# Performance work log

Measured on AMD Instinct MI355X. Metric: run time of the kernel, lower is better.

The kernel has to match this reference:

```python
import jax, jax.numpy as jnp
import numpy as np

E = 1024   # embd_size
H = 16     # heads_num
DH = E // H
DFF = 4 * E
B, T = 2, 2048


def layer_norm(x, g, b, eps=1e-5):
    mu = jnp.mean(x, axis=-1, keepdims=True)
    var = jnp.var(x, axis=-1, keepdims=True)
    return (x - mu) * jax.lax.rsqrt(var + eps) * g + b


def setup_inputs() -> dict:
    key = jax.random.key(0)
    ks = jax.random.split(key, 12)
    s = 0.02
    return {
        "x": jax.random.normal(ks[0], (B, T, E), dtype=jnp.float32),
        "Wq": jax.random.normal(ks[1], (E, E), dtype=jnp.float32) * s,
        "Wk": jax.random.normal(ks[2], (E, E), dtype=jnp.float32) * s,
        "Wv": jax.random.normal(ks[3], (E, E), dtype=jnp.float32) * s,
        "Wo": jax.random.normal(ks[4], (E, E), dtype=jnp.float32) * s,
        "bo": jnp.zeros((E,), dtype=jnp.float32),
        "W1": jax.random.normal(ks[5], (E, DFF), dtype=jnp.float32) * s,
        "b1": jnp.zeros((DFF,), dtype=jnp.float32),
        "W2": jax.random.normal(ks[6], (DFF, E), dtype=jnp.float32) * s,
        "b2": jnp.zeros((E,), dtype=jnp.float32),
        "g1": jnp.ones((E,), dtype=jnp.float32),
        "be1": jnp.zeros((E,), dtype=jnp.float32),
        "g2": jnp.ones((E,), dtype=jnp.float32),
        "be2": jnp.zeros((E,), dtype=jnp.float32),
    }


def reference(x, Wq, Wk, Wv, Wo, bo, W1, b1, W2, b2, g1, be1, g2, be2):
    Bx, Tx, C = x.shape
    # --- self-attention sublayer ---
    h = layer_norm(x, g1, be1)
    # per-head projections; heads concatenated along output dim == stacked weights
    q = (h @ Wq).reshape(Bx, Tx, H, DH)  # [B,T,H,Dh]
    k = (h @ Wk).reshape(Bx, Tx, H, DH)
    v = (h @ Wv).reshape(Bx, Tx, H, DH)
    # NOTE: original scales by full embd_size**-0.5 (C = x.shape[-1]), not head_size
    scale = C ** (-0.5)
    scores = jnp.einsum("bqhd,bkhd->bhqk", q, k) * scale  # [B,H,T,T]
    mask = jnp.tril(jnp.ones((Tx, Tx), dtype=bool))
    scores = jnp.where(mask, scores, -jnp.inf)
    attn = jax.nn.softmax(scores, axis=-1)
    o = jnp.einsum("bhqk,bkhd->bqhd", attn, v).reshape(Bx, Tx, C)
    sa = o @ Wo + bo
    x = x + sa
    # --- feed-forward sublayer ---
    h2 = layer_norm(x, g2, be2)
    ff = jax.nn.relu(h2 @ W1 + b1) @ W2 + b2
    return x + ff
```

## Files before the change

### kernel.cpp

```cpp
#include <hip/hip_runtime.h>
#include <hip/hip_bf16.h>
#include <math.h>

#define Bn 2
#define Tn 2048
#define En 1024
#define Hn 16
#define DFFn 4096
#define Mn (Bn*Tn)
#define QKVLD 3072

typedef __hip_bfloat16 bf16;
typedef unsigned short u16;
typedef unsigned int u32;
typedef __attribute__((ext_vector_type(8))) short short8;
typedef __attribute__((ext_vector_type(4))) float f32x4;

typedef __attribute__((address_space(1))) const void cg_void;
typedef __attribute__((address_space(3))) void lds_void;

#define QSC 0.0450842200278f

#define HBAR() asm volatile("s_waitcnt lgkmcnt(0)\n\ts_barrier" ::: "memory")

__device__ __forceinline__ u16 f2bf(float f) {
    bf16 h = __float2bfloat16(f);
    u16 u; __builtin_memcpy(&u, &h, 2); return u;
}
__device__ __forceinline__ float bf2f(u16 u) {
    u32 x = ((u32)u) << 16; float f; __builtin_memcpy(&f, &x, 4); return f;
}

__global__ __launch_bounds__(256)
void transpose_w4(const float* __restrict__ s0, const float* __restrict__ s1,
                  const float* __restrict__ s2, const float* __restrict__ s3,
                  u16* __restrict__ d0, u16* __restrict__ d1,
                  u16* __restrict__ d2, u16* __restrict__ d3) {
    const float* src = (blockIdx.z == 0) ? s0 : (blockIdx.z == 1) ? s1
                     : (blockIdx.z == 2) ? s2 : s3;
    u16* dst = (blockIdx.z == 0) ? d0 : (blockIdx.z == 1) ? d1
             : (blockIdx.z == 2) ? d2 : d3;
    __shared__ float t[64][65];
    const int r0 = blockIdx.y * 64, c0 = blockIdx.x * 64;
    const int tr = threadIdx.x >> 6, tc = threadIdx.x & 63;
#pragma unroll
    for (int i = 0; i < 16; i++)
        t[tr + i * 4][tc] = src[(size_t)(r0 + tr + i * 4) * 1024 + c0 + tc];
    __syncthreads();
#pragma unroll
    for (int i = 0; i < 16; i++)
        dst[(size_t)(c0 + tr + i * 4) * 1024 + r0 + tc] = f2bf(t[tc][tr + i * 4]);
}

__global__ __launch_bounds__(256)
void transpose_w(const float* __restrict__ src, u16* __restrict__ dst,
                 int R, int C) {
    __shared__ float t[64][65];
    const int r0 = blockIdx.y * 64, c0 = blockIdx.x * 64;
    const int tr = threadIdx.x >> 6, tc = threadIdx.x & 63;
#pragma unroll
    for (int i = 0; i < 16; i++)
        t[tr + i * 4][tc] = src[(size_t)(r0 + tr + i * 4) * C + c0 + tc];
    __syncthreads();
#pragma unroll
    for (int i = 0; i < 16; i++)
        dst[(size_t)(c0 + tr + i * 4) * R + r0 + tc] = f2bf(t[tc][tr + i * 4]);
}

__global__ __launch_bounds__(256)
void vcopy_t(const u16* __restrict__ QKV, u16* __restrict__ Vg) {
    const int bh = blockIdx.z;
    const int t0 = blockIdx.y * 64;
    __shared__ u16 t[64][65];
    const int tr = threadIdx.x >> 6, tc = threadIdx.x & 63;
    const u16* src = QKV + (size_t)(bh >> 4) * 2048 * QKVLD + 2048 + (bh & 15) * 64;
#pragma unroll
    for (int i = 0; i < 16; i++)
        t[tr + i * 4][tc] = src[(size_t)(t0 + tr + i * 4) * QKVLD + tc];
    __syncthreads();
    u16* dst = Vg + (size_t)bh * 64 * 2048;
#pragma unroll
    for (int i = 0; i < 16; i++)
        dst[(size_t)(tr + i * 4) * 2048 + t0 + tc] = t[tc][tr + i * 4];
}

template<typename AT>
__global__ __launch_bounds__(256)
void ln_kernel(const AT* __restrict__ x, const float* __restrict__ g,
               const float* __restrict__ b, u16* __restrict__ out) {
    const int row = blockIdx.x;
    const int tid = threadIdx.x;
    const AT* xp = x + (size_t)row * En;
    float v[4];
    float s = 0.f, sq = 0.f;
#pragma unroll
    for (int i = 0; i < 4; i++) {
        if constexpr (sizeof(AT) == 2) v[i] = bf2f(xp[tid + i * 256]);
        else                           v[i] = (float)xp[tid + i * 256];
        s += v[i];
        sq += v[i] * v[i];
    }
    __shared__ float rs[256], rq[256];
    rs[tid] = s; rq[tid] = sq;
    __syncthreads();
    for (int st = 128; st > 0; st >>= 1) {
        if (tid < st) { rs[tid] += rs[tid + st]; rq[tid] += rq[tid + st]; }
        __syncthreads();
    }
    const float mu  = rs[0] * (1.0f / En);
    const float var = rq[0] * (1.0f / En) - mu * mu;
    const float inv = rsqrtf(var + 1e-5f);
#pragma unroll
    for (int i = 0; i < 4; i++) {
        const int c = tid + i * 256;
        out[(size_t)row * En + c] = f2bf((v[i] - mu) * inv * g[c] + b[c]);
    }
}

__global__ __launch_bounds__(256)
void ff2_init(const u16* __restrict__ X1, const float* __restrict__ b2,
              float* __restrict__ out) {
    const int row = blockIdx.x;
    const int c = threadIdx.x * 4;
    ushort4 a = *(const ushort4*)&X1[(size_t)row * En + c];
    float4 bb = *(const float4*)&b2[c];
    float4 o;
    o.x = bf2f(a.x) + bb.x;
    o.y = bf2f(a.y) + bb.y;
    o.z = bf2f(a.z) + bb.z;
    o.w = bf2f(a.w) + bb.w;
    *(float4*)&out[(size_t)row * En + c] = o;
}

template<int TN, int HAS_BIAS, int RELU, int SPLITC, int SCQ, int ATOM,
         int SPLITA, int XSWZ>
__global__ __launch_bounds__(512, 2)
void gemm256(const u16* __restrict__ A, const u16* __restrict__ A2, int ldA,
             const u16* __restrict__ Wt, int ldW,
             const float* __restrict__ bias,
             u16* __restrict__ Cout, u16* __restrict__ Cout2,
             float* __restrict__ outF, int ldC, int Kd) {
    constexpr int WGN = (TN == 256) ? 4 : 2;
    constexpr int MF  = (256 / (8 / WGN)) / 16;
    constexpr int NF  = (TN / WGN) / 16;
    __shared__ __align__(16) u16 As[2][256 * 64];
    __shared__ __align__(16) u16 Bs[2][TN * 64];
    const int tid  = threadIdx.x;
    const int lane = tid & 63, wv = tid >> 6;
    const int quad = lane >> 4, l16 = lane & 15;
    const int wr = wv / WGN, wc = wv % WGN;
    const int lr8 = lane >> 3;
    const int gcg = (lane & 7) ^ lr8;

    int bx = blockIdx.x, by = blockIdx.y, bz = blockIdx.z;
    if (XSWZ) {
        const int GX = gridDim.x, GY = gridDim.y;
        const int L = (bz * GY + by) * GX + bx;
        const int xcd = L & 7, slot = L >> 3;
        const int p = slot / GX;
        bx = slot - p * GX;
        const int yz = p * 8 + xcd;
        by = yz & (GY - 1);
        bz = yz >> 4;
    }

    const int m0 = by * 256, n0 = bx * TN;
    const u16* Ap = (SPLITA && ATOM && bz) ? A2 : A;
    const int kbase = ATOM ? bz * Kd : 0;

    f32x4 acc[MF][NF] = {};

    auto stage = [&](int buf, int kt) {
#pragma unroll
        for (int i = 0; i < 4; i++) {
            const int rbase = wv * 32 + i * 8;
            __builtin_amdgcn_global_load_lds(
                (cg_void*)(const void*)&Ap[(size_t)(m0 + rbase + lr8) * ldA + kt + gcg * 8],
                (lds_void*)(void*)&As[buf][rbase * 64], 16, 0, 0);
        }
#pragma unroll
        for (int i = 0; i < TN / 64; i++) {
            const int rbase = wv * (TN / 8) + i * 8;
            __builtin_amdgcn_global_load_lds(
                (cg_void*)(const void*)&Wt[(size_t)(n0 + rbase + lr8) * ldW + kbase + kt + gcg * 8],
                (lds_void*)(void*)&Bs[buf][rbase * 64], 16, 0, 0);
        }
    };
    auto compute = [&](int buf) {
        const int swz = l16 & 7;
#pragma unroll
        for (int ks = 0; ks < 2; ks++) {
            short8 a[MF], b[NF];
#pragma unroll
            for (int mf = 0; mf < MF; mf++)
                a[mf] = *(const short8*)&As[buf][(wr * (MF * 16) + mf * 16 + l16) * 64 +
                         (((ks * 4 + quad) ^ swz) * 8)];
#pragma unroll
            for (int nf = 0; nf < NF; nf++)
                b[nf] = *(const short8*)&Bs[buf][(wc * 64 + nf * 16 + l16) * 64 +
                         (((ks * 4 + quad) ^ swz) * 8)];
#pragma unroll
            for (int mf = 0; mf < MF; mf++)
#pragma unroll
                for (int nf = 0; nf < NF; nf++)
                    acc[mf][nf] = __builtin_amdgcn_mfma_f32_16x16x32_bf16(
                        a[mf], b[nf], acc[mf][nf], 0, 0, 0);
        }
    };

    stage(0, 0);
    asm volatile("s_waitcnt vmcnt(0)" ::: "memory");
    __builtin_amdgcn_s_barrier();
    const int NT = Kd >> 6;
    for (int t = 0; t < NT; ++t) {
        const int cur = t & 1;
        if (t + 1 < NT) stage(cur ^ 1, (t + 1) * 64);
        compute(cur);
        asm volatile("s_waitcnt vmcnt(0) lgkmcnt(0)" ::: "memory");
        __builtin_amdgcn_s_barrier();
    }

    const float qscale = (SCQ && n0 < 1024) ? QSC : 1.0f;
#pragma unroll
    for (int mf = 0; mf < MF; mf++) {
#pragma unroll
        for (int r = 0; r < 4; r++) {
            const int gm = m0 + wr * (MF * 16) + mf * 16 + quad * 4 + r;
#pragma unroll
            for (int nf = 0; nf < NF; nf++) {
                const int gn = n0 + wc * 64 + nf * 16 + l16;
                const int cn = SPLITC ? (gn & 2047) : gn;
                float c = acc[mf][nf][r];
                if (HAS_BIAS) c += bias[gn];
                if (RELU) c = fmaxf(c, 0.f);
                if (SCQ) c *= qscale;
                if (ATOM) {
                    atomicAdd(&outF[(size_t)gm * ldC + gn], c);
                } else {
                    u16* Cp = (SPLITC && gn >= 2048) ? Cout2 : Cout;
                    Cp[(size_t)gm * ldC + cn] = f2bf(c);
                }
            }
        }
    }
}

template<int TM, int HAS_BIAS, int RELU, int RES, int OUT_F32, int SCQ,
         int SPLITC, int SPLITA, int ATOM = 0, int XSWZ = 0, int PIPE = 0>
__global__ __launch_bounds__(256)
void gemm_bt(const u16* __restrict__ A, const u16* __restrict__ A2, int ldA,
             const u16* __restrict__ Wt, int ldW,
             const float* __restrict__ bias, const void* __restrict__ res,
             void* __restrict__ Cout, void* __restrict__ Cout2,
             int ldC, int Kd) {
    constexpr int IF = TM / 32;
    constexpr int RB = 1;
    __shared__ __align__(16) u16 As[RB][TM * 32];
    __shared__ __align__(16) u16 Bs[RB][128 * 32];
    const int tid  = threadIdx.x;
    const int lane = tid & 63, wv = tid >> 6;
    const int quad = lane >> 4, l16 = lane & 15;

    int bx = blockIdx.x, by = blockIdx.y, bz = blockIdx.z;
    if (XSWZ) {
        const int GX = gridDim.x, GY = gridDim.y;
        const int L = (bz * GY + by) * GX + bx;
        const int xcd = L & 7, slot = L >> 3;
        const int p = slot / GX;
        bx = slot - p * GX;
        const int yz = p * 8 + xcd;
        by = yz & (GY - 1);
        bz = yz >> __builtin_ctz(GY);
    }

    const int m0 = by * TM, n0 = bx * 128;
    const int rw = (wv >> 1) * (TM / 2), cw = (wv & 1) * 64;
    const int lr  = lane >> 2;
    const int gsw = ((lane & 3) ^ ((lane >> 3) & 3)) * 8;
    const int psw = (quad ^ ((l16 >> 1) & 3)) * 8;

    f32x4 acc[IF][4] = {};

    auto stage = [&](int buf, int kt) {
        const u16* Ap = (SPLITA && kt >= 2048) ? A2 : A;
        const int  kk = SPLITA ? (kt & 2047) : kt;
#pragma unroll
        for (int t = 0; t < TM / 64; t++) {
            const int row = wv * (TM / 4) + t * 16;
            __builtin_amdgcn_global_load_lds(
                (cg_void*)(const void*)&Ap[(size_t)(m0 + row + lr) * ldA + kk + gsw],
                (lds_void*)(void*)&As[buf][row * 32], 16, 0, 0);
        }
#pragma unroll
        for (int t = 0; t < 2; t++) {
            const int row = wv * 32 + t * 16;
            __builtin_amdgcn_global_load_lds(
                (cg_void*)(const void*)&Wt[(size_t)(n0 + row + lr) * ldW + kt + gsw],
                (lds_void*)(void*)&Bs[buf][row * 32], 16, 0, 0);
        }
    };
    auto compute = [&](int buf) {
        short8 af[IF], bfr[4];
#pragma unroll
        for (int i = 0; i < IF; i++)
            af[i] = *(const short8*)&As[buf][(rw + i * 16 + l16) * 32 + psw];
#pragma unroll
        for (int j = 0; j < 4; j++)
            bfr[j] = *(const short8*)&Bs[buf][(cw + j * 16 + l16) * 32 + psw];
#pragma unroll
        for (int i = 0; i < IF; i++)
#pragma unroll
            for (int j = 0; j < 4; j++)
                acc[i][j] = __builtin_amdgcn_mfma_f32_16x16x32_bf16(
                    af[i], bfr[j], acc[i][j], 0, 0, 0);
    };

    const int kbase = ATOM ? bz * Kd : 0;
    for (int kt = kbase; kt < kbase + Kd; kt += 32) {
        __syncthreads();
        stage(0, kt);
        __syncthreads();
        compute(0);
    }

    const float qscale = (SCQ && n0 < 1024) ? QSC : 1.0f;
    void* Cp = (SPLITC && n0 >= 2048) ? Cout2 : Cout;
#pragma unroll
    for (int i = 0; i < IF; i++) {
#pragma unroll
        for (int r = 0; r < 4; r++) {
            const int gm = m0 + rw + i * 16 + quad * 4 + r;
#pragma unroll
            for (int j = 0; j < 4; j++) {
                const int gn = n0 + cw + j * 16 + l16;
                const int cn = SPLITC ? (gn & 2047) : gn;
                float c = acc[i][j][r];
                if (HAS_BIAS) c += bias[gn];
                if (RELU) c = fmaxf(c, 0.f);
                if (RES == 1) c += ((const float*)res)[(size_t)gm * ldC + cn];
                if (RES == 2) c += bf2f(((const u16*)res)[(size_t)gm * ldC + cn]);
                if (SCQ) c *= qscale;
                if (ATOM) {
                    atomicAdd(&((float*)Cp)[(size_t)gm * ldC + cn], c);
                } else if (OUT_F32) {
                    ((float*)Cp)[(size_t)gm * ldC + cn] = c;
                } else {
                    ((u16*)Cp)[(size_t)gm * ldC + cn] = f2bf(c);
                }
            }
        }
    }
}

__global__ __launch_bounds__(256)
void flash_pass1(const u16* __restrict__ QKV, const u16* __restrict__ Vg,
                 u16* __restrict__ Op0, u16* __restrict__ Op1qkv,
                 float* __restrict__ stats) {
    const int pr = blockIdx.x >> 1, half = blockIdx.x & 1;
    const int hh = blockIdx.y, bb = blockIdx.z;
    const int tid  = threadIdx.x;
    const int lane = tid & 63, wv = tid >> 6;
    const int quad = lane >> 4, l16 = lane & 15;

    __shared__ __align__(16) u16 Ks[2][64 * 64];
    __shared__ __align__(16) u16 Vt[2][64 * 64];
    __shared__ __align__(16) u16 Ps[4][16 * 64];

    const size_t rowbase = (size_t)(bb * Tn) * QKVLD;
    const u16* Vgh = Vg + (size_t)(bb * Hn + hh) * 64 * 2048;

    const int sr = tid >> 2;
    const int p0 = (tid & 3) | ((sr & 1) << 2);
    const int p1 = p0 ^ 4;
    const int g0 = p0 ^ (sr & 7), g1 = p1 ^ (sr & 7);
    const int lsw = l16 & 7;

    uint4 kA, kB, vA, vB;
    auto prefetch = [&](int kt) {
        const size_t kb = rowbase + (size_t)(kt * 64 + sr) * QKVLD + 1024 + hh * 64;
        kA = *(const uint4*)&QKV[kb + g0 * 8];
        kB = *(const uint4*)&QKV[kb + g1 * 8];
        const size_t vb = (size_t)sr * 2048 + kt * 64;
        vA = *(const uint4*)&Vgh[vb + g0 * 8];
        vB = *(const uint4*)&Vgh[vb + g1 * 8];
    };
    auto writebuf = [&](int buf) {
        *(uint4*)&Ks[buf][sr * 64 + p0 * 8] = kA;
        *(uint4*)&Ks[buf][sr * 64 + p1 * 8] = kB;
        *(uint4*)&Vt[buf][sr * 64 + p0 * 8] = vA;
        *(uint4*)&Vt[buf][sr * 64 + p1 * 8] = vB;
    };

    for (int qsel = 0; qsel < 2; qsel++) {
        const int qt = qsel ? (31 - pr) : pr;
        const int nk = (qt >= half) ? ((qt - half) >> 1) + 1 : 0;
        const int qrow = qt * 64 + wv * 16 + l16;
        const int grow = bb * Tn + qrow;

        f32x4 ot[4] = {};
        float m2 = -INFINITY, lrow = 0.f;

        HBAR();
        if (nk > 0) {
            const u16* qp = QKV + rowbase + (size_t)qrow * QKVLD + hh * 64;
            short8 qf[2];
            qf[0] = *(const short8*)&qp[quad * 8];
            qf[1] = *(const short8*)&qp[32 + quad * 8];

            prefetch(half);
            writebuf(0);
            if (nk > 1) prefetch(half + 2);
            HBAR();

            const bool hasdiag = ((qt ^ half) & 1) == 0;
            for (int f = 0; f < nk; f++) {
                const int cur = f & 1;

                f32x4 st[4] = {};
#pragma unroll
                for (int ks = 0; ks < 2; ks++)
#pragma unroll
                    for (int i = 0; i < 4; i++) {
                        short8 kf = *(const short8*)&Ks[cur][(i * 16 + l16) * 64 +
                                     (((ks * 4 + quad) ^ lsw) * 8)];
                        st[i] = __builtin_amdgcn_mfma_f32_16x16x32_bf16(
                            kf, qf[ks], st[i], 0, 0, 0);
                    }

                float tmax = -INFINITY;
                if (hasdiag && f == nk - 1) {
                    const int qloc = wv * 16 + l16;
#pragma unroll
                    for (int i = 0; i < 4; i++)
#pragma unroll
                        for (int r = 0; r < 4; r++) {
                            float s = st[i][r];
                            if (i * 16 + quad * 4 + r > qloc) s = -INFINITY;
                            st[i][r] = s;
                            tmax = fmaxf(tmax, s);
                        }
                } else {
#pragma unroll
                    for (int i = 0; i < 4; i++)
#pragma unroll
                        for (int r = 0; r < 4; r++)
                            tmax = fmaxf(tmax, st[i][r]);
                }
                tmax = fmaxf(tmax, __shfl_xor(tmax, 16));
                tmax = fmaxf(tmax, __shfl_xor(tmax, 32));

                const float mnew = fmaxf(m2, tmax);
                const float alpha = exp2f(m2 - mnew);
                m2 = mnew;
                float psum = 0.f;
#pragma unroll
                for (int i = 0; i < 4; i++)
#pragma unroll
                    for (int r = 0; r < 4; r++) {
                        const float e = exp2f(st[i][r] - mnew);
                        st[i][r] = e;
                        psum += e;
                    }
                psum += __shfl_xor(psum, 16);
                psum += __shfl_xor(psum, 32);
                lrow = lrow * alpha + psum;
#pragma unroll
                for (int i = 0; i < 4; i++) ot[i] *= alpha;

#pragma unroll
                for (int i = 0; i < 4; i++) {
                    uint2 w;
                    w.x = (u32)f2bf(st[i][0]) | ((u32)f2bf(st[i][1]) << 16);
                    w.y = (u32)f2bf(st[i][2]) | ((u32)f2bf(st[i][3]) << 16);
                    const int g = (i * 2 + (quad >> 1)) ^ lsw;
                    *(uint2*)&Ps[wv][l16 * 64 + g * 8 + (quad & 1) * 4] = w;
                }
                asm volatile("s_waitcnt lgkmcnt(0)" ::: "memory");

#pragma unroll
                for (int ks = 0; ks < 2; ks++) {
                    short8 pf = *(const short8*)&Ps[wv][l16 * 64 +
                                 (((ks * 4 + quad) ^ lsw) * 8)];
#pragma unroll
                    for (int i = 0; i < 4; i++) {
                        short8 vf = *(const short8*)&Vt[cur][(i * 16 + l16) * 64 +
                                     (((ks * 4 + quad) ^ lsw) * 8)];
                        ot[i] = __builtin_amdgcn_mfma_f32_16x16x32_bf16(
                            vf, pf, ot[i], 0, 0, 0);
                    }
                }

                if (f + 1 < nk) {
                    writebuf(cur ^ 1);
                    if (f + 2 < nk) prefetch(half + 2 * (f + 2));
                    HBAR();
                }
            }
        }

        u16* op = (half == 0) ? (Op0 + (size_t)grow * 1024 + hh * 64)
                              : (Op1qkv + (size_t)grow * QKVLD + 2048 + hh * 64);
#pragma unroll
        for (int i = 0; i < 4; i++) {
            ushort4 o4;
            o4.x = f2bf(ot[i][0]); o4.y = f2bf(ot[i][1]);
            o4.z = f2bf(ot[i][2]); o4.w = f2bf(ot[i][3]);
            *(ushort4*)&op[i * 16 + quad * 4] = o4;
        }
        if (quad == 0) {
            stats[((size_t)(half * 2 + 0) * 4096 + grow) * 16 + hh] = m2;
            stats[((size_t)(half * 2 + 1) * 4096 + grow) * 16 + hh] = lrow;
        }
    }
}

__global__ __launch_bounds__(256)
void flash_merge(u16* __restrict__ QKV, const u16* __restrict__ Op0,
                 const float* __restrict__ stats) {
    const int row = blockIdx.x;
    const int tid = threadIdx.x;
    const int col = tid * 4;
    const int hh = col >> 6;
    const float m0 = stats[((size_t)0 * 4096 + row) * 16 + hh];
    const float l0 = stats[((size_t)1 * 4096 + row) * 16 + hh];
    const float m1 = stats[((size_t)2 * 4096 + row) * 16 + hh];
    const float l1 = stats[((size_t)3 * 4096 + row) * 16 + hh];
    const float m  = fmaxf(m0, m1);
    const float w0 = exp2f(m0 - m), w1 = exp2f(m1 - m);
    const float inv = 1.0f / (w0 * l0 + w1 * l1);
    ushort4 a = *(const ushort4*)&Op0[(size_t)row * 1024 + col];
    ushort4 b = *(const ushort4*)&QKV[(size_t)row * QKVLD + 2048 + col];
    ushort4 o;
    o.x = f2bf((w0 * bf2f(a.x) + w1 * bf2f(b.x)) * inv);
    o.y = f2bf((w0 * bf2f(a.y) + w1 * bf2f(b.y)) * inv);
    o.z = f2bf((w0 * bf2f(a.z) + w1 * bf2f(b.z)) * inv);
    o.w = f2bf((w0 * bf2f(a.w) + w1 * bf2f(b.w)) * inv);
    *(ushort4*)&QKV[(size_t)row * QKVLD + col] = o;
}

extern "C" void kernel_launch(void* const* d_in, const int* in_sizes, int n_in,
                              void* d_out, int out_size, void* d_ws, size_t ws_size,
                              hipStream_t stream) {
    const float* x   = (const float*)d_in[0];
    const float* Wq  = (const float*)d_in[1];
    const float* Wk  = (const float*)d_in[2];
    const float* Wv  = (const float*)d_in[3];
    const float* Wo  = (const float*)d_in[4];
    const float* bo  = (const float*)d_in[5];
    const float* W1  = (const float*)d_in[6];
    const float* b1  = (const float*)d_in[7];
    const float* W2  = (const float*)d_in[8];
    const float* b2  = (const float*)d_in[9];
    const float* g1  = (const float*)d_in[10];
    const float* be1 = (const float*)d_in[11];
    const float* g2  = (const float*)d_in[12];
    const float* be2 = (const float*)d_in[13];

    char* wsb = (char*)d_ws;
    u16*   QKV = (u16*)wsb;
    u16*   F1a = (u16*)wsb;
    u16*   W2T = (u16*)(wsb + 16u * 1024 * 1024);
    u16*   Op0 = (u16*)(wsb + 24u * 1024 * 1024);
    u16*   X1b = Op0;
    u16*   Vg  = (u16*)(wsb + 32u * 1024 * 1024);
    u16*   F1b = Vg;
    u16*   h     = (u16*)d_out;
    u16*   WT    = (u16*)((char*)d_out + 8u * 1024 * 1024);
    u16*   WqkvT = WT;
    u16*   WoT   = WT + 3u * 1024 * 1024;
    float* stats = (float*)WT;
    u16*   W1T   = WT;

    transpose_w4<<<dim3(16, 16, 4), 256, 0, stream>>>(
        Wq, Wk, Wv, Wo,
        WqkvT, WqkvT + 1024u * 1024, WqkvT + 2048u * 1024, WoT);

    ln_kernel<float><<<Mn, 256, 0, stream>>>(x, g1, be1, h);

    gemm256<256, 0, 0, 0, 1, 0, 0, 1><<<dim3(12, 16), 512, 0, stream>>>(
        h, nullptr, En, WqkvT, En, nullptr, QKV, nullptr, nullptr, QKVLD, En);

    vcopy_t<<<dim3(1, 32, 32), 256, 0, stream>>>(QKV, Vg);

    flash_pass1<<<dim3(32, Hn, Bn), 256, 0, stream>>>(QKV, Vg, Op0, QKV, stats);

    flash_merge<<<Mn, 256, 0, stream>>>(QKV, Op0, stats);

    gemm_bt<64, 1, 0, 1, 0, 0, 0, 0, 0, 1, 0><<<dim3(8, 64), 256, 0, stream>>>(
        QKV, nullptr, QKVLD, WoT, En, bo, x, X1b, nullptr, En, En);

    transpose_w<<<dim3(64, 16), 256, 0, stream>>>(W1, W1T, 1024, 4096);
    transpose_w<<<dim3(16, 64), 256, 0, stream>>>(W2, W2T, 4096, 1024);

    ln_kernel<u16><<<Mn, 256, 0, stream>>>(X1b, g2, be2, h);

    gemm256<256, 1, 1, 1, 0, 0, 0, 1><<<dim3(16, 16), 512, 0, stream>>>(
        h, nullptr, En, W1T, En, b1, F1a, F1b, nullptr, 2048, En);

    ff2_init<<<Mn, 256, 0, stream>>>(X1b, b2, (float*)d_out);

    gemm256<128, 0, 0, 0, 0, 1, 1, 1><<<dim3(8, 16, 2), 512, 0, stream>>>(
        F1a, F1b, 2048, W2T, DFFn, nullptr, nullptr, nullptr,
        (float*)d_out, En, 2048);
}
```

Before: 366.8 us.

## Deepen GEMM pipeline to 4-stage K=32 ring with partial vmcnt waits

Restructures the GEMM main loop from a double-buffered K=64 tile to a 4-deep ring of K=32 tiles, prefetching three stages ahead and waiting with counted vmcnt so loads stay in flight across iterations. The LDS layout and XOR swizzle change to 32-element rows, and compute is wrapped in s_setprio to favour MFMA issue. The goal is to hide global-to-LDS latency better. In exchange there are twice as many barriers per K step and fragile hand-counted wait values.

```diff
diff --git a/kernel.cpp b/kernel.cpp
--- a/kernel.cpp
+++ b/kernel.cpp
@@ -143,14 +143,15 @@
     constexpr int WGN = (TN == 256) ? 4 : 2;
     constexpr int MF  = (256 / (8 / WGN)) / 16;
     constexpr int NF  = (TN / WGN) / 16;
-    __shared__ __align__(16) u16 As[2][256 * 64];
-    __shared__ __align__(16) u16 Bs[2][TN * 64];
+    constexpr int LD  = 2 + TN / 128;
+    __shared__ __align__(16) u16 As[4][256 * 32];
+    __shared__ __align__(16) u16 Bs[4][TN * 32];
     const int tid  = threadIdx.x;
     const int lane = tid & 63, wv = tid >> 6;
     const int quad = lane >> 4, l16 = lane & 15;
     const int wr = wv / WGN, wc = wv % WGN;
-    const int lr8 = lane >> 3;
-    const int gcg = (lane & 7) ^ lr8;
+    const int lr4 = lane >> 2;
+    const int gcg = (lane & 3) ^ (lr4 & 3);
 
     int bx = blockIdx.x, by = blockIdx.y, bz = blockIdx.z;
     if (XSWZ) {
@@ -172,51 +173,68 @@
 
     auto stage = [&](int buf, int kt) {
 #pragma unroll
-        for (int i = 0; i < 4; i++) {
-            const int rbase = wv * 32 + i * 8;
+        for (int i = 0; i < 2; i++) {
+            const int rbase = i * 128 + wv * 16;
             __builtin_amdgcn_global_load_lds(
-                (cg_void*)(const void*)&Ap[(size_t)(m0 + rbase + lr8) * ldA + kt + gcg * 8],
-                (lds_void*)(void*)&As[buf][rbase * 64], 16, 0, 0);
-        }
-#pragma unroll
-        for (int i = 0; i < TN / 64; i++) {
-            const int rbase = wv * (TN / 8) + i * 8;
+                (cg_void*)(const void*)&Ap[(size_t)(m0 + rbase + lr4) * ldA + kt + gcg * 8],
+                (lds_void*)(void*)&As[buf][rbase * 32], 16, 0, 0);
+        }
+#pragma unroll
+        for (int i = 0; i < TN / 128; i++) {
+            const int rbase = i * 128 + wv * 16;
             __builtin_amdgcn_global_load_lds(
-                (cg_void*)(const void*)&Wt[(size_t)(n0 + rbase + lr8) * ldW + kbase + kt + gcg * 8],
-                (lds_void*)(void*)&Bs[buf][rbase * 64], 16, 0, 0);
+                (cg_void*)(const void*)&Wt[(size_t)(n0 + rbase + lr4) * ldW + kbase + kt + gcg * 8],
+                (lds_void*)(void*)&Bs[buf][rbase * 32], 16, 0, 0);
         }
     };
     auto compute = [&](int buf) {
-        const int swz = l16 & 7;
-#pragma unroll
-        for (int ks = 0; ks < 2; ks++) {
-            short8 a[MF], b[NF];
-#pragma unroll
-            for (int mf = 0; mf < MF; mf++)
-                a[mf] = *(const short8*)&As[buf][(wr * (MF * 16) + mf * 16 + l16) * 64 +
-                         (((ks * 4 + quad) ^ swz) * 8)];
+        const int swz = l16 & 3;
+        short8 a[MF], b[NF];
+#pragma unroll
+        for (int mf = 0; mf < MF; mf++)
+            a[mf] = *(const short8*)&As[buf][(wr * (MF * 16) + mf * 16 + l16) * 32 +
+                     ((quad ^ swz) * 8)];
+#pragma unroll
+        for (int nf = 0; nf < NF; nf++)
+            b[nf] = *(const short8*)&Bs[buf][(wc * 64 + nf * 16 + l16) * 32 +
+                     ((quad ^ swz) * 8)];
+#pragma unroll
+        for (int mf = 0; mf < MF; mf++)
 #pragma unroll
             for (int nf = 0; nf < NF; nf++)
-                b[nf] = *(const short8*)&Bs[buf][(wc * 64 + nf * 16 + l16) * 64 +
-                         (((ks * 4 + quad) ^ swz) * 8)];
-#pragma unroll
-            for (int mf = 0; mf < MF; mf++)
-#pragma unroll
-                for (int nf = 0; nf < NF; nf++)
-                    acc[mf][nf] = __builtin_amdgcn_mfma_f32_16x16x32_bf16(
-                        a[mf], b[nf], acc[mf][nf], 0, 0, 0);
-        }
+                acc[mf][nf] = __builtin_amdgcn_mfma_f32_16x16x32_bf16(
+                    a[mf], b[nf], acc[mf][nf], 0, 0, 0);
     };
 
+    const int NH = Kd >> 5;
     stage(0, 0);
-    asm volatile("s_waitcnt vmcnt(0)" ::: "memory");
-    __builtin_amdgcn_s_barrier();
-    const int NT = Kd >> 6;
-    for (int t = 0; t < NT; ++t) {
-        const int cur = t & 1;
-        if (t + 1 < NT) stage(cur ^ 1, (t + 1) * 64);
-        compute(cur);
-        asm volatile("s_waitcnt vmcnt(0) lgkmcnt(0)" ::: "memory");
+    stage(1, 32);
+    stage(2, 64);
+    int bc = 0, bs = 3;
+    for (int it = 0; it < NH; ++it) {
+        if (it + 3 < NH) {
+            stage(bs, (it + 3) * 32);
+            if (++bs == 4) bs = 0;
+        }
+        const int rem = (NH - 1 - it) < 3 ? (NH - 1 - it) : 3;
+        if (rem == 3) {
+            if constexpr (LD == 4) asm volatile("s_waitcnt vmcnt(12)" ::: "memory");
+            else                   asm volatile("s_waitcnt vmcnt(9)"  ::: "memory");
+        } else if (rem == 2) {
+            if constexpr (LD == 4) asm volatile("s_waitcnt vmcnt(8)"  ::: "memory");
+            else                   asm volatile("s_waitcnt vmcnt(6)"  ::: "memory");
+        } else if (rem == 1) {
+            if constexpr (LD == 4) asm volatile("s_waitcnt vmcnt(4)"  ::: "memory");
+            else                   asm volatile("s_waitcnt vmcnt(3)"  ::: "memory");
+        } else {
+            asm volatile("s_waitcnt vmcnt(0)" ::: "memory");
+        }
+        __builtin_amdgcn_s_barrier();
+        __builtin_amdgcn_s_setprio(1);
+        compute(bc);
+        __builtin_amdgcn_s_setprio(0);
+        if (++bc == 4) bc = 0;
+        asm volatile("s_waitcnt lgkmcnt(0)" ::: "memory");
         __builtin_amdgcn_s_barrier();
     }
 
```

Measured after the change: 401.4 us. 9.4% more time.
